# Performance work log

Measured on AMD Instinct MI355X. Metric: run time of the kernel, lower is better.

Reference implementation:

```python
import jax, jax.numpy as jnp
import numpy as np

EPS = 1e-5


def conv1x1(x, w):
    # x: (N, C, V, T), w: (O, C) -> (N, O, V, T)
    return jnp.einsum('ncvt,oc->novt', x, w)


def batchnorm2d(y, gamma, beta):
    # training-mode BN over (N, V, T) per channel, biased variance (torch semantics)
    mean = jnp.mean(y, axis=(0, 2, 3), keepdims=True)
    var = jnp.mean((y - mean) ** 2, axis=(0, 2, 3), keepdims=True)
    yhat = (y - mean) * jax.lax.rsqrt(var + EPS)
    return yhat * gamma[None, :, None, None] + beta[None, :, None, None]


def spatial_g(x, wg1, wg2):
    # learned adjacency: softmax over last dim of (N, T, V, V)
    a1 = conv1x1(x, wg1)  # (N, O, V, T)
    a2 = conv1x1(x, wg2)  # (N, O, V, T)
    g = jnp.einsum('novt,nout->ntvu', a1, a2)  # (N, T, V, V)
    return jax.nn.softmax(g, axis=-1)


def gcn_unit(x, g, w1, w2, gamma, beta):
    # message passing: g (N,T,V,V) applied over joint dim of x (N,C,V,T)
    x1 = jnp.einsum('ntvu,ncut->ncvt', g, x)
    y = conv1x1(x1, w1) + conv1x1(x, w2)
    return jax.nn.relu(batchnorm2d(y, gamma, beta))


def setup_inputs() -> dict:
    key = jax.random.key(0)
    ks = jax.random.split(key, 12)
    N, C, V, T = 64, 64, 25, 128
    dims = [64, 64, 128, 256]
    gp = 16
    s = 0.05
    inp = {
        'x': jax.random.normal(ks[0], (N, C, V, T), jnp.float32),
        'wg1': jax.random.normal(ks[1], (gp, dims[0]), jnp.float32) * s,
        'wg2': jax.random.normal(ks[2], (gp, dims[0]), jnp.float32) * s,
        'w11': jax.random.normal(ks[3], (dims[1], dims[0]), jnp.float32) * s,
        'w12': jax.random.normal(ks[4], (dims[1], dims[0]), jnp.float32) * s,
        'gamma1': jnp.ones((dims[1],), jnp.float32),
        'beta1': jnp.zeros((dims[1],), jnp.float32),
        'w21': jax.random.normal(ks[5], (dims[2], dims[1]), jnp.float32) * s,
        'w22': jax.random.normal(ks[6], (dims[2], dims[1]), jnp.float32) * s,
        'gamma2': jnp.ones((dims[2],), jnp.float32),
        'beta2': jnp.zeros((dims[2],), jnp.float32),
        'w31': jax.random.normal(ks[7], (dims[3], dims[2]), jnp.float32) * s,
        'w32': jax.random.normal(ks[8], (dims[3], dims[2]), jnp.float32) * s,
        'gamma3': jnp.ones((dims[3],), jnp.float32),
        'beta3': jnp.zeros((dims[3],), jnp.float32),
    }
    return inp


def reference(x, wg1, wg2, w11, w12, gamma1, beta1, w21, w22, gamma2, beta2,
              w31, w32, gamma3, beta3):
    g = spatial_g(x, wg1, wg2)                       # shared adjacency (N,T,V,V)
    x = gcn_unit(x, g, w11, w12, gamma1, beta1)      # (N, 64, V, T)
    x = gcn_unit(x, g, w21, w22, gamma2, beta2)      # (N, 128, V, T)
    x = gcn_unit(x, g, w31, w32, gamma3, beta3)      # (N, 256, V, T)
    return x, g
```

## Files before the change

### kernel.cpp

```cpp
#include <hip/hip_runtime.h>
#include <cstdint>

#define V_ 25
#define T_ 128
#define VT_ 3200
#define NVTF_ 204800.0f

typedef unsigned short ushort_t;
typedef __attribute__((ext_vector_type(8))) short s16x8;
typedef __attribute__((ext_vector_type(4))) float f32x4;

__device__ __forceinline__ ushort_t f2bf(float f) {
    union { float f; unsigned u; } v; v.f = f;
    unsigned r = v.u + 0x7FFFu + ((v.u >> 16) & 1u);
    return (ushort_t)(r >> 16);
}
__device__ __forceinline__ float bf2f(ushort_t h) {
    union { unsigned u; float f; } v; v.u = ((unsigned)h) << 16;
    return v.f;
}
__device__ __forceinline__ void gload16(const void* g, void* l) {
    __builtin_amdgcn_global_load_lds((const __attribute__((address_space(1))) void*)g,
                                     (__attribute__((address_space(3))) void*)l, 16, 0, 0);
}

__global__ __launch_bounds__(128) void k_a(const float* __restrict__ x,
        const float* __restrict__ wg1, const float* __restrict__ wg2,
        ushort_t* __restrict__ a1, ushort_t* __restrict__ a2,
        ushort_t* __restrict__ xb) {
    int b = blockIdx.x; int n = b / V_; int v = b % V_;
    int t = threadIdx.x;
    __shared__ float w1s[1024], w2s[1024];
    for (int i = threadIdx.x; i < 1024; i += 128) { w1s[i] = wg1[i]; w2s[i] = wg2[i]; }
    __syncthreads();
    float s1[16], s2[16];
    #pragma unroll
    for (int o = 0; o < 16; o++) { s1[o] = 0.f; s2[o] = 0.f; }
    s16x8 xs[8];
    const float* xp = x + (size_t)n * 204800 + v * T_ + t;
    #pragma unroll
    for (int c = 0; c < 64; c++) {
        float xv = xp[(size_t)c * VT_];
        xs[c >> 3][c & 7] = (short)f2bf(xv);
        #pragma unroll
        for (int o = 0; o < 16; o++) {
            s1[o] = fmaf(w1s[o*64+c], xv, s1[o]);
            s2[o] = fmaf(w2s[o*64+c], xv, s2[o]);
        }
    }
    size_t abase = (size_t)n * 51200 + v * T_ + t;
    #pragma unroll
    for (int o = 0; o < 16; o++) {
        a1[abase + (size_t)o * VT_] = f2bf(s1[o]);
        a2[abase + (size_t)o * VT_] = f2bf(s2[o]);
    }
    ushort_t* cp = xb + (size_t)(n * VT_ + v * T_ + t) * 64;
    #pragma unroll
    for (int ch = 0; ch < 8; ch++) *(s16x8*)(cp + ch * 8) = xs[ch];
}

__global__ __launch_bounds__(256) void k_g(const ushort_t* __restrict__ a1,
        const ushort_t* __restrict__ a2, float* __restrict__ g,
        ushort_t* __restrict__ gb) {
    int n = blockIdx.x >> 3; int t0 = (blockIdx.x & 7) * 16;
    __shared__ float A1s[6400], A2s[6400];
    for (int i = threadIdx.x; i < 6400; i += 256) {
        int o = i / 400; int r = i % 400; int v = r >> 4; int tt = r & 15;
        size_t ga = (size_t)n * 51200 + (size_t)o * VT_ + v * T_ + t0 + tt;
        A1s[i] = bf2f(a1[ga]);
        A2s[i] = bf2f(a2[ga]);
    }
    __syncthreads();
    for (int r = threadIdx.x; r < 400; r += 256) {
        int v = r >> 4; int tt = r & 15;
        float a1r[16];
        #pragma unroll
        for (int o = 0; o < 16; o++) a1r[o] = A1s[o*400 + v*16 + tt];
        float gr[25];
        float mx = -1e30f;
        for (int u = 0; u < 25; u++) {
            float s = 0.f;
            #pragma unroll
            for (int o = 0; o < 16; o++) s = fmaf(a1r[o], A2s[o*400 + u*16 + tt], s);
            gr[u] = s; mx = fmaxf(mx, s);
        }
        float sum = 0.f;
        for (int u = 0; u < 25; u++) { gr[u] = __expf(gr[u] - mx); sum += gr[u]; }
        float inv = 1.f / sum;
        float* gp = g + ((size_t)(n * T_ + t0 + tt) * V_ + v) * V_;
        ushort_t* gbp = gb + ((size_t)((n * 128 + t0 + tt) * 25 + v)) * 32;
        for (int u = 0; u < 25; u++) {
            float val = gr[u] * inv;
            gp[u] = val;
            gbp[u] = f2bf(val);
        }
    }
}

__global__ void k_wcat(const float* __restrict__ w11, const float* __restrict__ w12,
        const float* __restrict__ w21, const float* __restrict__ w22,
        const float* __restrict__ w31, const float* __restrict__ w32,
        ushort_t* __restrict__ Wc) {
    int i = blockIdx.x * 256 + threadIdx.x;
    float v;
    if (i < 8192) {
        int o = i >> 7, k = i & 127;
        v = (k < 64) ? w11[o * 64 + k] : w12[o * 64 + k - 64];
    } else if (i < 24576) {
        int j = i - 8192; int o = j >> 7, k = j & 127;
        v = (k < 64) ? w21[o * 64 + k] : w22[o * 64 + k - 64];
    } else {
        int j = i - 24576; int o = j >> 8, k = j & 255;
        v = (k < 128) ? w31[o * 128 + k] : w32[o * 128 + k - 128];
    }
    Wc[i] = f2bf(v);
}

template<int C, bool BNB, bool XBSRC, int TOUT, int OPASS>
__global__ __launch_bounds__(256) void k_fgemm(
        const ushort_t* __restrict__ Wc, const ushort_t* __restrict__ ysrc,
        const ushort_t* __restrict__ gb,
        const float* __restrict__ bns, const float* __restrict__ bnb,
        ushort_t* __restrict__ yt,
        float* __restrict__ psum, float* __restrict__ psq) {
    constexpr int K2 = 2 * C;
    constexpr int KSTEPS = K2 / 32;
    constexpr int NC8 = C / 8;
    constexpr int HKS = C / 32;
    constexpr int MROWS = 100;
    constexpr int MI = 7;
    constexpr int CW = (C == 64) ? 1 : 2;
    constexpr int XBYTES = (TOUT == 0) ? 14400 : 11200;
    __shared__ __align__(16) ushort_t YS[MROWS * C];
    __shared__ __align__(16) ushort_t MPo[MROWS * C];
    __shared__ __align__(16) char XTRA[XBYTES];
    float* GS = (float*)XTRA;
    ushort_t* Lw = (ushort_t*)XTRA;

    int n = blockIdx.y, mb = blockIdx.x;
    int m0 = mb * MROWS, tb = mb * 4;
    int tid = threadIdx.x, w = tid >> 6, lane = tid & 63;
    int l15 = lane & 15, g4 = lane >> 4;

    for (int i = tid; i < 2500; i += 256) {
        int tl = i / 625, r = i % 625, u = r / 25, v = r % 25;
        GS[(tl * 25 + u) * 28 + v] =
            bf2f(gb[((size_t)((n * 128 + tb + tl) * 25 + v)) * 32 + u]);
    }
    for (int i = tid; i < MROWS * NC8; i += 256) {
        int yr = i / NC8, cc = i % NC8;
        size_t saddr;
        if (XBSRC) {
            int t = tb + yr / 25, v = yr % 25;
            saddr = (size_t)n * 204800 + (size_t)(v * 128 + t) * 64 + cc * 8;
        } else {
            saddr = ((size_t)n * VT_ + m0 + yr) * C + cc * 8;
        }
        s16x8 vv = *(const s16x8*)(ysrc + saddr);
        if (BNB) {
            int ob = cc * 8;
            float4 s0 = *(const float4*)(bns + ob), s1 = *(const float4*)(bns + ob + 4);
            float4 h0 = *(const float4*)(bnb + ob), h1 = *(const float4*)(bnb + ob + 4);
            float sc[8] = {s0.x, s0.y, s0.z, s0.w, s1.x, s1.y, s1.z, s1.w};
            float sh[8] = {h0.x, h0.y, h0.z, h0.w, h1.x, h1.y, h1.z, h1.w};
            #pragma unroll
            for (int j = 0; j < 8; j++) {
                float f = fmaf(bf2f((ushort_t)vv[j]), sc[j], sh[j]);
                vv[j] = (short)f2bf(fmaxf(f, 0.f));
            }
        }
        *(s16x8*)(YS + ((size_t)yr * NC8 + (cc ^ (yr & 7))) * 8) = vv;
    }
    __syncthreads();
    {
        int cwi = tid & 63;
        int tl = tid >> 6;
        int c8 = (cwi * CW) >> 3;
        int sub = (cwi * CW) & 7;
        float macc[25][CW];
        #pragma unroll
        for (int v = 0; v < 25; v++)
            #pragma unroll
            for (int k = 0; k < CW; k++) macc[v][k] = 0.f;
        for (int u = 0; u < 25; u++) {
            int yr = tl * 25 + u;
            const ushort_t* yp = YS + ((size_t)yr * NC8 + (c8 ^ (yr & 7))) * 8 + sub;
            float yf[CW];
            if (CW == 2) {
                unsigned yw = *(const unsigned*)yp;
                yf[0] = bf2f((ushort_t)(yw & 0xFFFFu));
                yf[1] = bf2f((ushort_t)(yw >> 16));
            } else {
                yf[0] = bf2f(*yp);
            }
            const float* gp = &GS[(tl * 25 + u) * 28];
            float gv[25];
            #pragma unroll
            for (int q = 0; q < 6; q++) {
                float4 gq = *(const float4*)(gp + q * 4);
                gv[q*4+0] = gq.x; gv[q*4+1] = gq.y; gv[q*4+2] = gq.z; gv[q*4+3] = gq.w;
            }
            gv[24] = gp[24];
            #pragma unroll
            for (int v = 0; v < 25; v++)
                #pragma unroll
                for (int k = 0; k < CW; k++)
                    macc[v][k] = fmaf(gv[v], yf[k], macc[v][k]);
        }
        #pragma unroll
        for (int v = 0; v < 25; v++) {
            int r = tl * 25 + v;
            ushort_t* op = MPo + ((size_t)r * NC8 + (c8 ^ (r & 7))) * 8 + sub;
            if (CW == 2) {
                unsigned w2 = (unsigned)f2bf(macc[v][0]) | ((unsigned)f2bf(macc[v][1]) << 16);
                *(unsigned*)op = w2;
            } else {
                *op = f2bf(macc[v][0]);
            }
        }
    }
    __syncthreads();
    for (int pass = 0; pass < OPASS; pass++) {
        int o0 = pass * 64;
        s16x8 aReg[KSTEPS];
        const ushort_t* ap = Wc + (size_t)(o0 + w * 16 + l15) * K2 + g4 * 8;
        #pragma unroll
        for (int ks = 0; ks < KSTEPS; ks++)
            aReg[ks] = *(const s16x8*)(ap + ks * 32);
        f32x4 acc[MI] = {};
        __builtin_amdgcn_s_setprio(1);
        #pragma unroll
        for (int ks = 0; ks < KSTEPS; ks++) {
            const ushort_t* bbase = (ks < HKS) ? MPo : YS;
            int ksl = (ks < HKS) ? ks : ks - HKS;
            #pragma unroll
            for (int mi = 0; mi < MI; mi++) {
                int r = mi * 16 + l15;
                int rr = (r < MROWS) ? r : (MROWS - 1);
                int ch = ksl * 4 + g4;
                s16x8 bF = *(const s16x8*)(bbase + ((size_t)rr * NC8 + (ch ^ (rr & 7))) * 8);
                acc[mi] = __builtin_amdgcn_mfma_f32_16x16x32_bf16(aReg[ks], bF, acc[mi], 0, 0, 0);
            }
        }
        __builtin_amdgcn_s_setprio(0);
        int p = n * 32 + mb;
        #pragma unroll
        for (int b = 0; b < 4; b++) {
            float ss = 0.f, qq = 0.f;
            #pragma unroll
            for (int mi = 0; mi < MI; mi++) {
                float v0 = acc[mi][b];
                if (mi == 6 && l15 >= 4) v0 = 0.f;
                ss += v0; qq = fmaf(v0, v0, qq);
            }
            #pragma unroll
            for (int msk = 1; msk < 16; msk <<= 1) {
                ss += __shfl_xor(ss, msk, 16);
                qq += __shfl_xor(qq, msk, 16);
            }
            if (l15 == 0) {
                int o = o0 + w * 16 + g4 * 4 + b;
                psum[(size_t)o * 2048 + p] = ss;
                psq [(size_t)o * 2048 + p] = qq;
            }
        }
        if (TOUT == 0) {
            __syncthreads();
            #pragma unroll
            for (int mi = 0; mi < MI; mi++) {
                int r = mi * 16 + l15;
                if (r < MROWS) {
                    #pragma unroll
                    for (int b = 0; b < 4; b++)
                        Lw[r * 72 + w * 16 + g4 * 4 + b] = f2bf(acc[mi][b]);
                }
            }
            __syncthreads();
            for (int i = tid; i < MROWS * 8; i += 256) {
                int r = i >> 3, oc = i & 7;
                s16x8 pk = *(const s16x8*)(Lw + r * 72 + oc * 8);
                *(s16x8*)(yt + ((size_t)n * VT_ + m0 + r) * (OPASS * 64) + o0 + oc * 8) = pk;
            }
        } else {
            int obase = n * 256 + o0 + w * 16 + g4 * 4;
            #pragma unroll
            for (int mi = 0; mi < MI; mi++) {
                int r = mi * 16 + l15;
                if (r < MROWS) {
                    #pragma unroll
                    for (int b = 0; b < 4; b++)
                        yt[(size_t)(obase + b) * VT_ + m0 + r] = f2bf(acc[mi][b]);
                }
            }
        }
    }
}

__global__ __launch_bounds__(256) void k_stats(const float* __restrict__ psum,
        const float* __restrict__ psq, const float* __restrict__ gamma,
        const float* __restrict__ beta, float* __restrict__ bns,
        float* __restrict__ bnb) {
    int o = blockIdx.x;
    float s = 0.f, q = 0.f;
    for (int i = threadIdx.x; i < 2048; i += 256) {
        s += psum[(size_t)o*2048+i]; q += psq[(size_t)o*2048+i];
    }
    __shared__ float rs[256], rq[256];
    rs[threadIdx.x] = s; rq[threadIdx.x] = q;
    __syncthreads();
    for (int st = 128; st > 0; st >>= 1) {
        if (threadIdx.x < st) { rs[threadIdx.x] += rs[threadIdx.x+st]; rq[threadIdx.x] += rq[threadIdx.x+st]; }
        __syncthreads();
    }
    if (threadIdx.x == 0) {
        float mean = rs[0] / NVTF_;
        float var = rq[0] / NVTF_ - mean * mean;
        float scale = gamma[o] * rsqrtf(var + 1e-5f);
        bns[o] = scale;
        bnb[o] = beta[o] - mean * scale;
    }
}

__global__ __launch_bounds__(256) void k_bnf(const ushort_t* __restrict__ y3,
        const float* __restrict__ bns, const float* __restrict__ bnb,
        float* __restrict__ xout) {
    __shared__ __align__(16) ushort_t L[8 * VT_];
    int n = blockIdx.y, oc = blockIdx.x;
    size_t base = (size_t)(n * 256 + oc * 8) * VT_;
    for (int i = threadIdx.x; i < 3200; i += 256)
        gload16(y3 + base + (size_t)i * 8, (char*)L + i * 16);
    __syncthreads();
    for (int i = threadIdx.x; i < 6400; i += 256) {
        int t4 = i & 31, v = (i >> 5) % 25, o = i / 800;
        int og = oc * 8 + o;
        float sc = bns[og], sh = bnb[og];
        int lb = o * VT_ + v;
        float4 f;
        f.x = fmaxf(fmaf(bf2f(L[lb + (t4*4+0)*25]), sc, sh), 0.f);
        f.y = fmaxf(fmaf(bf2f(L[lb + (t4*4+1)*25]), sc, sh), 0.f);
        f.z = fmaxf(fmaf(bf2f(L[lb + (t4*4+2)*25]), sc, sh), 0.f);
        f.w = fmaxf(fmaf(bf2f(L[lb + (t4*4+3)*25]), sc, sh), 0.f);
        *(float4*)(xout + (size_t)(n * 256 + og) * VT_ + v * T_ + t4 * 4) = f;
    }
}

extern "C" void kernel_launch(void* const* d_in, const int* in_sizes, int n_in,
                              void* d_out, int out_size, void* d_ws, size_t ws_size,
                              hipStream_t stream) {
    const float* x   = (const float*)d_in[0];
    const float* wg1 = (const float*)d_in[1];
    const float* wg2 = (const float*)d_in[2];
    const float* w11 = (const float*)d_in[3];
    const float* w12 = (const float*)d_in[4];
    const float* ga1 = (const float*)d_in[5];
    const float* be1 = (const float*)d_in[6];
    const float* w21 = (const float*)d_in[7];
    const float* w22 = (const float*)d_in[8];
    const float* ga2 = (const float*)d_in[9];
    const float* be2 = (const float*)d_in[10];
    const float* w31 = (const float*)d_in[11];
    const float* w32 = (const float*)d_in[12];
    const float* ga3 = (const float*)d_in[13];
    const float* be3 = (const float*)d_in[14];

    float* xout = (float*)d_out;
    float* gout = xout + 52428800;

    float* ws = (float*)d_ws;
    ushort_t* xb  = (ushort_t*)(ws + 0);
    ushort_t* a1  = (ushort_t*)(ws + 6553600);
    ushort_t* a2  = (ushort_t*)(ws + 8192000);
    ushort_t* y1  = (ushort_t*)(ws + 9830400);
    ushort_t* y2  = (ushort_t*)(ws + 16384000);
    ushort_t* y3  = (ushort_t*)(ws + 29491200);
    ushort_t* gb  = (ushort_t*)(ws + 55705600);
    float* psum = ws + 58982400;
    float* psq  = ws + 59506688;
    ushort_t* Wc = (ushort_t*)(ws + 60030976);
    float* bns  = ws + 60076032;
    float* bnb  = ws + 60076288;
    ushort_t* Wc1 = Wc, *Wc2 = Wc + 8192, *Wc3 = Wc + 24576;

    k_a<<<1600, 128, 0, stream>>>(x, wg1, wg2, a1, a2, xb);
    k_g<<<512, 256, 0, stream>>>(a1, a2, gout, gb);
    k_wcat<<<352, 256, 0, stream>>>(w11, w12, w21, w22, w31, w32, Wc);

    k_fgemm<64, false, true, 0, 1><<<dim3(32, 64), 256, 0, stream>>>(
        Wc1, xb, gb, nullptr, nullptr, y1, psum, psq);
    k_stats<<<64, 256, 0, stream>>>(psum, psq, ga1, be1, bns, bnb);

    k_fgemm<64, true, false, 0, 2><<<dim3(32, 64), 256, 0, stream>>>(
        Wc2, y1, gb, bns, bnb, y2, psum, psq);
    k_stats<<<128, 256, 0, stream>>>(psum, psq, ga2, be2, bns, bnb);

    k_fgemm<128, true, false, 2, 4><<<dim3(32, 64), 256, 0, stream>>>(
        Wc3, y2, gb, bns, bnb, y3, psum, psq);
    k_stats<<<256, 256, 0, stream>>>(psum, psq, ga3, be3, bns, bnb);

    k_bnf<<<dim3(32, 64), 256, 0, stream>>>(y3, bns, bnb, xout);
}
```

Before: 341.1 us.

## Fold weight concat into k_a, use packed bf16 converts, stage transposed stores

Merges the weight-concatenation kernel into the first projection kernel, which removes one launch. Replaces software float-to-bf16 rounding with the hardware v_cvt_pk_bf16_f32 packed convert at several sites. In the layer-3 GEMM, the transposed output is now staged through LDS so it can be written as 8-byte vector stores instead of scattered 2-byte stores. This adds two barriers and a slightly larger LDS scratch buffer.

```diff
diff --git a/kernel.cpp b/kernel.cpp
--- a/kernel.cpp
+++ b/kernel.cpp
@@ -8,6 +8,7 @@
 
 typedef unsigned short ushort_t;
 typedef __attribute__((ext_vector_type(8))) short s16x8;
+typedef __attribute__((ext_vector_type(4))) short s16x4;
 typedef __attribute__((ext_vector_type(4))) float f32x4;
 
 __device__ __forceinline__ ushort_t f2bf(float f) {
@@ -19,6 +20,11 @@
     union { unsigned u; float f; } v; v.u = ((unsigned)h) << 16;
     return v.f;
 }
+__device__ __forceinline__ unsigned cvtpk(float lo, float hi) {
+    unsigned r;
+    asm volatile("v_cvt_pk_bf16_f32 %0, %1, %2" : "=v"(r) : "v"(lo), "v"(hi));
+    return r;
+}
 __device__ __forceinline__ void gload16(const void* g, void* l) {
     __builtin_amdgcn_global_load_lds((const __attribute__((address_space(1))) void*)g,
                                      (__attribute__((address_space(3))) void*)l, 16, 0, 0);
@@ -27,9 +33,28 @@
 __global__ __launch_bounds__(128) void k_a(const float* __restrict__ x,
         const float* __restrict__ wg1, const float* __restrict__ wg2,
         ushort_t* __restrict__ a1, ushort_t* __restrict__ a2,
-        ushort_t* __restrict__ xb) {
+        ushort_t* __restrict__ xb,
+        const float* __restrict__ w11, const float* __restrict__ w12,
+        const float* __restrict__ w21, const float* __restrict__ w22,
+        const float* __restrict__ w31, const float* __restrict__ w32,
+        ushort_t* __restrict__ Wc) {
     int b = blockIdx.x; int n = b / V_; int v = b % V_;
     int t = threadIdx.x;
+    int wi = b * 128 + t;
+    if (wi < 90112) {
+        float wv;
+        if (wi < 8192) {
+            int o = wi >> 7, k = wi & 127;
+            wv = (k < 64) ? w11[o * 64 + k] : w12[o * 64 + k - 64];
+        } else if (wi < 24576) {
+            int j = wi - 8192; int o = j >> 7, k = j & 127;
+            wv = (k < 64) ? w21[o * 64 + k] : w22[o * 64 + k - 64];
+        } else {
+            int j = wi - 24576; int o = j >> 8, k = j & 255;
+            wv = (k < 128) ? w31[o * 128 + k] : w32[o * 128 + k - 128];
+        }
+        Wc[wi] = f2bf(wv);
+    }
     __shared__ float w1s[1024], w2s[1024];
     for (int i = threadIdx.x; i < 1024; i += 128) { w1s[i] = wg1[i]; w2s[i] = wg2[i]; }
     __syncthreads();
@@ -95,25 +120,6 @@
             gbp[u] = f2bf(val);
         }
     }
-}
-
-__global__ void k_wcat(const float* __restrict__ w11, const float* __restrict__ w12,
-        const float* __restrict__ w21, const float* __restrict__ w22,
-        const float* __restrict__ w31, const float* __restrict__ w32,
-        ushort_t* __restrict__ Wc) {
-    int i = blockIdx.x * 256 + threadIdx.x;
-    float v;
-    if (i < 8192) {
-        int o = i >> 7, k = i & 127;
-        v = (k < 64) ? w11[o * 64 + k] : w12[o * 64 + k - 64];
-    } else if (i < 24576) {
-        int j = i - 8192; int o = j >> 7, k = j & 127;
-        v = (k < 64) ? w21[o * 64 + k] : w22[o * 64 + k - 64];
-    } else {
-        int j = i - 24576; int o = j >> 8, k = j & 255;
-        v = (k < 128) ? w31[o * 128 + k] : w32[o * 128 + k - 128];
-    }
-    Wc[i] = f2bf(v);
 }
 
 template<int C, bool BNB, bool XBSRC, int TOUT, int OPASS>
@@ -130,7 +136,7 @@
     constexpr int MROWS = 100;
     constexpr int MI = 7;
     constexpr int CW = (C == 64) ? 1 : 2;
-    constexpr int XBYTES = (TOUT == 0) ? 14400 : 11200;
+    constexpr int XBYTES = (TOUT == 0) ? 14400 : 13824;
     __shared__ __align__(16) ushort_t YS[MROWS * C];
     __shared__ __align__(16) ushort_t MPo[MROWS * C];
     __shared__ __align__(16) char XTRA[XBYTES];
@@ -163,11 +169,14 @@
             float4 h0 = *(const float4*)(bnb + ob), h1 = *(const float4*)(bnb + ob + 4);
             float sc[8] = {s0.x, s0.y, s0.z, s0.w, s1.x, s1.y, s1.z, s1.w};
             float sh[8] = {h0.x, h0.y, h0.z, h0.w, h1.x, h1.y, h1.z, h1.w};
-            #pragma unroll
-            for (int j = 0; j < 8; j++) {
-                float f = fmaf(bf2f((ushort_t)vv[j]), sc[j], sh[j]);
-                vv[j] = (short)f2bf(fmaxf(f, 0.f));
-            }
+            float ff[8];
+            #pragma unroll
+            for (int j = 0; j < 8; j++)
+                ff[j] = fmaxf(fmaf(bf2f((ushort_t)vv[j]), sc[j], sh[j]), 0.f);
+            union { unsigned u[4]; s16x8 s; } U;
+            U.u[0] = cvtpk(ff[0], ff[1]); U.u[1] = cvtpk(ff[2], ff[3]);
+            U.u[2] = cvtpk(ff[4], ff[5]); U.u[3] = cvtpk(ff[6], ff[7]);
+            vv = U.s;
         }
         *(s16x8*)(YS + ((size_t)yr * NC8 + (cc ^ (yr & 7))) * 8) = vv;
     }
@@ -212,8 +221,7 @@
             int r = tl * 25 + v;
             ushort_t* op = MPo + ((size_t)r * NC8 + (c8 ^ (r & 7))) * 8 + sub;
             if (CW == 2) {
-                unsigned w2 = (unsigned)f2bf(macc[v][0]) | ((unsigned)f2bf(macc[v][1]) << 16);
-                *(unsigned*)op = w2;
+                *(unsigned*)op = cvtpk(macc[v][0], macc[v][1]);
             } else {
                 *op = f2bf(macc[v][0]);
             }
@@ -270,9 +278,10 @@
             for (int mi = 0; mi < MI; mi++) {
                 int r = mi * 16 + l15;
                 if (r < MROWS) {
-                    #pragma unroll
-                    for (int b = 0; b < 4; b++)
-                        Lw[r * 72 + w * 16 + g4 * 4 + b] = f2bf(acc[mi][b]);
+                    unsigned lo = cvtpk(acc[mi][0], acc[mi][1]);
+                    unsigned hi = cvtpk(acc[mi][2], acc[mi][3]);
+                    *(unsigned*)(Lw + r * 72 + w * 16 + g4 * 4)     = lo;
+                    *(unsigned*)(Lw + r * 72 + w * 16 + g4 * 4 + 2) = hi;
                 }
             }
             __syncthreads();
@@ -282,15 +291,23 @@
                 *(s16x8*)(yt + ((size_t)n * VT_ + m0 + r) * (OPASS * 64) + o0 + oc * 8) = pk;
             }
         } else {
-            int obase = n * 256 + o0 + w * 16 + g4 * 4;
+            __syncthreads();
             #pragma unroll
             for (int mi = 0; mi < MI; mi++) {
                 int r = mi * 16 + l15;
                 if (r < MROWS) {
-                    #pragma unroll
-                    for (int b = 0; b < 4; b++)
-                        yt[(size_t)(obase + b) * VT_ + m0 + r] = f2bf(acc[mi][b]);
+                    int ol = w * 16 + g4 * 4;
+                    Lw[(ol + 0) * 108 + r] = f2bf(acc[mi][0]);
+                    Lw[(ol + 1) * 108 + r] = f2bf(acc[mi][1]);
+                    Lw[(ol + 2) * 108 + r] = f2bf(acc[mi][2]);
+                    Lw[(ol + 3) * 108 + r] = f2bf(acc[mi][3]);
                 }
+            }
+            __syncthreads();
+            for (int i = tid; i < 64 * 25; i += 256) {
+                int ol = i / 25, mc = i % 25;
+                s16x4 pk = *(const s16x4*)(Lw + ol * 108 + mc * 4);
+                *(s16x4*)(yt + (size_t)(n * 256 + o0 + ol) * VT_ + m0 + mc * 4) = pk;
             }
         }
     }
@@ -381,9 +398,9 @@
     float* bnb  = ws + 60076288;
     ushort_t* Wc1 = Wc, *Wc2 = Wc + 8192, *Wc3 = Wc + 24576;
 
-    k_a<<<1600, 128, 0, stream>>>(x, wg1, wg2, a1, a2, xb);
+    k_a<<<1600, 128, 0, stream>>>(x, wg1, wg2, a1, a2, xb,
+                                  w11, w12, w21, w22, w31, w32, Wc);
     k_g<<<512, 256, 0, stream>>>(a1, a2, gout, gb);
-    k_wcat<<<352, 256, 0, stream>>>(w11, w12, w21, w22, w31, w32, Wc);
 
     k_fgemm<64, false, true, 0, 1><<<dim3(32, 64), 256, 0, stream>>>(
         Wc1, xb, gb, nullptr, nullptr, y1, psum, psq);
```

New measurement: 347.8 us. No clear change (+2.0%).
